# Kernel tuning notes

Measured on AMD Instinct MI355X. Metric: run time of the kernel, lower is better.

The kernel has to match this reference:

```python
import jax, jax.numpy as jnp
from jax import lax
import numpy as np

P, K1, K2 = 8, 5, 9  # nPaths, small/large ECA kernel sizes (from nDim=1024, nPaths=8)
LN_EPS = 1e-5


def setup_inputs() -> dict:
    key = jax.random.key(0)
    ks = jax.random.split(key, 6)
    b, c, l = 16, 1024, 4096
    return {
        "x": jax.random.normal(ks[0], (b, c, l), dtype=jnp.float32),
        "conv1_w": jax.random.normal(ks[1], (P, K1), dtype=jnp.float32) * 0.3,
        "conv2_w": jax.random.normal(ks[2], (P, K2), dtype=jnp.float32) * 0.3,
        "combine_w": jax.random.normal(ks[3], (2,), dtype=jnp.float32) * 0.5,
        "combine_b": jnp.zeros((), dtype=jnp.float32),
        "ln_g": jnp.ones((P,), dtype=jnp.float32),
        "ln_b": jnp.zeros((P,), dtype=jnp.float32),
        "W1": jax.random.normal(ks[4], (P, 2 * P), dtype=jnp.float32) * 0.3,
        "b1": jnp.zeros((2 * P,), dtype=jnp.float32),
        "W2": jax.random.normal(ks[5], (2 * P, P), dtype=jnp.float32) * 0.3,
        "b2": jnp.zeros((P,), dtype=jnp.float32),
    }


def _grouped_conv(y, w):
    # y: (b, P, D) pooled per-path features; w: (P, k) one 1-ch kernel per path.
    # Equivalent to the per-path Conv1d(1,1,k, padding=(k-1)//2) loop, fused.
    k = w.shape[-1]
    pad = (k - 1) // 2
    return lax.conv_general_dilated(
        y, w[:, None, :], window_strides=(1,), padding=[(pad, pad)],
        dimension_numbers=("NCH", "OIH", "NCH"), feature_group_count=y.shape[1])


def reference(x, conv1_w, conv2_w, combine_w, combine_b, ln_g, ln_b, W1, b1, W2, b2):
    b, c, l = x.shape
    nP = conv1_w.shape[0]
    D = c // nP
    pf = x.reshape(b, nP, D, l)          # (b, P, D, l)
    y = pf.mean(-1)                      # (b, P, D) global-avg-pool over l
    y1 = _grouped_conv(y, conv1_w)       # (b, P, D)
    y2 = _grouped_conv(y, conv2_w)       # (b, P, D)
    # combine = Conv1d(2,1,1): scalar mix of the two conv outputs + bias
    attn = jax.nn.sigmoid(combine_w[0] * y1 + combine_w[1] * y2 + combine_b)
    # cross-path gating MLP on per-path mean attention
    cross = attn.mean(-1)                # (b, P)
    mu = cross.mean(-1, keepdims=True)
    var = cross.var(-1, keepdims=True)   # biased, matches torch LayerNorm
    h = (cross - mu) / jnp.sqrt(var + LN_EPS) * ln_g + ln_b
    h = jax.nn.gelu(h @ W1 + b1, approximate=False)
    gate = jax.nn.sigmoid(h @ W2 + b2)   # (b, P)
    scale = attn * gate[:, :, None]      # (b, P, D)
    out = pf * scale[..., None]          # broadcast over l
    return out.reshape(b, c, l)
```

## Files before the change

kernel.cpp:

```cpp
#include <hip/hip_runtime.h>
#include <math.h>

#define NP 8
#define ND 128
#define NC 1024
#define NL 4096
#define NB 16
#define LN_EPS 1e-5f

#define NBLK 2048
#define NCHUNK 8
#define GRPS 64

typedef float v4f __attribute__((ext_vector_type(4)));

__device__ __forceinline__ float hsum(v4f v) { return v.x + v.y + v.z + v.w; }
__device__ __forceinline__ float sigmoid_f(float z) { return 1.f / (1.f + expf(-z)); }

__device__ __forceinline__ float gelu_f(float s) {
    const float t = 0.7978845608028654f * (s + 0.044715f * s * s * s);
    const float e = expf(2.f * t);
    return 0.5f * s * (1.f + (e - 1.f) / (e + 1.f));
}

__global__ __launch_bounds__(256, 8) void fused_kernel(
    const float* __restrict__ x, float* __restrict__ y,
    unsigned* __restrict__ garr, unsigned* __restrict__ root,
    const float* __restrict__ conv1_w, const float* __restrict__ conv2_w,
    const float* __restrict__ combine_w, const float* __restrict__ combine_b,
    const float* __restrict__ ln_g, const float* __restrict__ ln_b,
    const float* __restrict__ W1, const float* __restrict__ b1,
    const float* __restrict__ W2, const float* __restrict__ b2,
    float* __restrict__ out)
{
    const int tid = threadIdx.x;
    const int bid = blockIdx.x;
    const int grp = bid >> 5;

    __shared__ float sred[4];
    __shared__ float sy[NC];
    __shared__ float sattn[NC];
    __shared__ float scross[NP];
    __shared__ float sh[NP];
    __shared__ float sh2[2 * NP];
    __shared__ float sgate[NP];
    __shared__ float sml[2];

    for (int c = 0; c < NCHUNK; ++c) {
        const int rowc = c * NBLK + bid;
        const int b    = rowc >> 10;
        const int ch0  = rowc & (NC - 1);
        const v4f* xb  = (const v4f*)x + (size_t)rowc * (NL / 4);
        v4f* ob        = (v4f*)out    + (size_t)rowc * (NL / 4);

        v4f a0 = xb[tid], a1 = xb[tid + 256], a2 = xb[tid + 512], a3 = xb[tid + 768];
        {
            float ps = hsum(a0) + hsum(a1) + hsum(a2) + hsum(a3);
            ps += __shfl_down(ps, 32, 64); ps += __shfl_down(ps, 16, 64);
            ps += __shfl_down(ps, 8, 64);  ps += __shfl_down(ps, 4, 64);
            ps += __shfl_down(ps, 2, 64);  ps += __shfl_down(ps, 1, 64);
            if ((tid & 63) == 0) sred[tid >> 6] = ps;
        }
        __syncthreads();
        if (tid == 0) {
            y[rowc] = (sred[0] + sred[1] + sred[2] + sred[3]) * (1.f / NL);
            __threadfence();
            unsigned old = __hip_atomic_fetch_add(&garr[grp], 1u,
                              __ATOMIC_RELEASE, __HIP_MEMORY_SCOPE_AGENT);
            if (old == (unsigned)(c * 32 + 31))
                __hip_atomic_fetch_add(root, 1u,
                              __ATOMIC_RELEASE, __HIP_MEMORY_SCOPE_AGENT);
            while (__hip_atomic_load(root, __ATOMIC_ACQUIRE,
                                     __HIP_MEMORY_SCOPE_AGENT) < (unsigned)((c + 1) * GRPS))
                __builtin_amdgcn_s_sleep(2);
        }
        __syncthreads();

        const float* yb = y + b * NC;
        #pragma unroll
        for (int k = 0; k < 4; ++k) {
            const int i = tid + 256 * k;
            sy[i] = __hip_atomic_load(&yb[i], __ATOMIC_RELAXED, __HIP_MEMORY_SCOPE_AGENT);
        }
        __syncthreads();
        #pragma unroll
        for (int k = 0; k < 4; ++k) {
            const int pos = tid + 256 * k;
            const int p = pos >> 7, d = pos & 127;
            const float* rowp = sy + p * ND;
            float c1 = 0.f;
            #pragma unroll
            for (int t = 0; t < 5; ++t) {
                int dd = d + t - 2;
                float v = (dd >= 0 && dd < ND) ? rowp[dd] : 0.f;
                c1 += conv1_w[p * 5 + t] * v;
            }
            float c2 = 0.f;
            #pragma unroll
            for (int t = 0; t < 9; ++t) {
                int dd = d + t - 4;
                float v = (dd >= 0 && dd < ND) ? rowp[dd] : 0.f;
                c2 += conv2_w[p * 9 + t] * v;
            }
            sattn[pos] = sigmoid_f(combine_w[0] * c1 + combine_w[1] * c2 + combine_b[0]);
        }
        __syncthreads();
        if (tid < 128) {
            const int p = tid >> 4, o = (tid & 15) * 8;
            float s = 0.f;
            #pragma unroll
            for (int j = 0; j < 8; ++j) s += sattn[p * ND + o + j];
            s += __shfl_down(s, 8, 16); s += __shfl_down(s, 4, 16);
            s += __shfl_down(s, 2, 16); s += __shfl_down(s, 1, 16);
            if ((tid & 15) == 0) scross[p] = s * (1.f / ND);
        }
        __syncthreads();
        if (tid == 0) {
            float mu = 0.f;
            #pragma unroll
            for (int pp = 0; pp < NP; ++pp) mu += scross[pp];
            mu *= (1.f / NP);
            float var = 0.f;
            #pragma unroll
            for (int pp = 0; pp < NP; ++pp) { float dl = scross[pp] - mu; var += dl * dl; }
            sml[0] = mu;
            sml[1] = rsqrtf(var * (1.f / NP) + LN_EPS);
        }
        __syncthreads();
        if (tid < NP)
            sh[tid] = (scross[tid] - sml[0]) * sml[1] * ln_g[tid] + ln_b[tid];
        __syncthreads();
        if (tid < 2 * NP) {
            float s = b1[tid];
            #pragma unroll
            for (int pp = 0; pp < NP; ++pp) s += sh[pp] * W1[pp * (2 * NP) + tid];
            sh2[tid] = gelu_f(s);
        }
        __syncthreads();
        if (tid < NP) {
            float s = b2[tid];
            #pragma unroll
            for (int j = 0; j < 2 * NP; ++j) s += sh2[j] * W2[j * NP + tid];
            sgate[tid] = sigmoid_f(s);
        }
        __syncthreads();

        const float s = sattn[ch0] * sgate[ch0 >> 7];
        __builtin_nontemporal_store(a0 * s, &ob[tid]);
        __builtin_nontemporal_store(a1 * s, &ob[tid + 256]);
        __builtin_nontemporal_store(a2 * s, &ob[tid + 512]);
        __builtin_nontemporal_store(a3 * s, &ob[tid + 768]);
        __syncthreads();
    }
}

__global__ __launch_bounds__(256) void pool_kernel(const float* __restrict__ x,
                                                   float* __restrict__ y) {
    const int wid  = threadIdx.x >> 6;
    const int lane = threadIdx.x & 63;
    const int row  = blockIdx.x * 4 + wid;
    const v4f* xr = (const v4f*)(x + (size_t)row * NL);
    float s = 0.f;
    #pragma unroll
    for (int i = 0; i < 16; ++i) {
        v4f v = xr[lane + i * 64];
        s += v.x + v.y + v.z + v.w;
    }
    #pragma unroll
    for (int off = 32; off; off >>= 1) s += __shfl_down(s, off, 64);
    if (lane == 0) y[row] = s * (1.f / NL);
}

__global__ __launch_bounds__(1024) void attn_kernel(
    const float* __restrict__ y,
    const float* __restrict__ conv1_w, const float* __restrict__ conv2_w,
    const float* __restrict__ combine_w, const float* __restrict__ combine_b,
    const float* __restrict__ ln_g, const float* __restrict__ ln_b,
    const float* __restrict__ W1, const float* __restrict__ b1,
    const float* __restrict__ W2, const float* __restrict__ b2,
    float* __restrict__ scale)
{
    const int b = blockIdx.x;
    const int tid = threadIdx.x;
    const int p = tid >> 7;
    const int d = tid & 127;

    __shared__ float sy[NC];
    __shared__ float sattn[NC];
    __shared__ float sred[16];
    __shared__ float scross[NP];
    __shared__ float sh[NP];
    __shared__ float sh2[2 * NP];
    __shared__ float sgate[NP];
    __shared__ float sml[2];

    sy[tid] = y[b * NC + tid];
    __syncthreads();

    const float* rowp = sy + p * ND;
    float c1 = 0.f;
    #pragma unroll
    for (int t = 0; t < 5; ++t) {
        int dd = d + t - 2;
        float v = (dd >= 0 && dd < ND) ? rowp[dd] : 0.f;
        c1 += conv1_w[p * 5 + t] * v;
    }
    float c2 = 0.f;
    #pragma unroll
    for (int t = 0; t < 9; ++t) {
        int dd = d + t - 4;
        float v = (dd >= 0 && dd < ND) ? rowp[dd] : 0.f;
        c2 += conv2_w[p * 9 + t] * v;
    }
    const float a = sigmoid_f(combine_w[0] * c1 + combine_w[1] * c2 + combine_b[0]);
    sattn[tid] = a;

    float r = a;
    #pragma unroll
    for (int off = 32; off; off >>= 1) r += __shfl_down(r, off, 64);
    const int lane = tid & 63, wid = tid >> 6;
    if (lane == 0) sred[wid] = r;
    __syncthreads();

    if (tid == 0) {
        float mu = 0.f, var = 0.f;
        #pragma unroll
        for (int pp = 0; pp < NP; ++pp) {
            scross[pp] = (sred[2 * pp] + sred[2 * pp + 1]) * (1.f / ND);
            mu += scross[pp];
        }
        mu *= (1.f / NP);
        #pragma unroll
        for (int pp = 0; pp < NP; ++pp) { float dl = scross[pp] - mu; var += dl * dl; }
        sml[0] = mu;
        sml[1] = rsqrtf(var * (1.f / NP) + LN_EPS);
    }
    __syncthreads();
    if (tid < NP)
        sh[tid] = (scross[tid] - sml[0]) * sml[1] * ln_g[tid] + ln_b[tid];
    __syncthreads();
    if (tid < 2 * NP) {
        float s = b1[tid];
        #pragma unroll
        for (int pp = 0; pp < NP; ++pp) s += sh[pp] * W1[pp * (2 * NP) + tid];
        sh2[tid] = gelu_f(s);
    }
    __syncthreads();
    if (tid < NP) {
        float s = b2[tid];
        #pragma unroll
        for (int j = 0; j < 2 * NP; ++j) s += sh2[j] * W2[j * NP + tid];
        sgate[tid] = sigmoid_f(s);
    }
    __syncthreads();

    scale[b * NC + tid] = sattn[tid] * sgate[p];
}

__global__ __launch_bounds__(256) void scale_kernel(const float* __restrict__ x,
                                                    const float* __restrict__ scale,
                                                    float* __restrict__ out) {
    const v4f* xv = (const v4f*)x;
    v4f* ov = (v4f*)out;
    const size_t n = (size_t)NB * NC * (NL / 4);
    const size_t stride = (size_t)gridDim.x * blockDim.x;
    for (size_t i = (size_t)blockIdx.x * blockDim.x + threadIdx.x; i < n; i += stride) {
        const float s = scale[i >> 10];
        v4f v = xv[i];
        v *= s;
        __builtin_nontemporal_store(v, &ov[i]);
    }
}

extern "C" void kernel_launch(void* const* d_in, const int* in_sizes, int n_in,
                              void* d_out, int out_size, void* d_ws, size_t ws_size,
                              hipStream_t stream) {
    const float* x         = (const float*)d_in[0];
    const float* conv1_w   = (const float*)d_in[1];
    const float* conv2_w   = (const float*)d_in[2];
    const float* combine_w = (const float*)d_in[3];
    const float* combine_b = (const float*)d_in[4];
    const float* ln_g      = (const float*)d_in[5];
    const float* ln_b      = (const float*)d_in[6];
    const float* W1        = (const float*)d_in[7];
    const float* b1        = (const float*)d_in[8];
    const float* W2        = (const float*)d_in[9];
    const float* b2        = (const float*)d_in[10];
    float* out = (float*)d_out;

    float* y        = (float*)d_ws;
    float* scale    = y + NB * NC;
    unsigned* garr  = (unsigned*)(void*)(((char*)d_ws) + (NB * NC) * sizeof(float));
    unsigned* root  = garr + GRPS;

    hipMemsetAsync((void*)garr, 0, (GRPS + 16) * sizeof(unsigned), stream);

    int nb = 0;
    hipOccupancyMaxActiveBlocksPerMultiprocessor(&nb, fused_kernel, 256, 0);
    if (nb >= NBLK / 256) {
        void* args[] = { (void*)&x, (void*)&y, (void*)&garr, (void*)&root,
                         (void*)&conv1_w, (void*)&conv2_w,
                         (void*)&combine_w, (void*)&combine_b,
                         (void*)&ln_g, (void*)&ln_b,
                         (void*)&W1, (void*)&b1, (void*)&W2, (void*)&b2,
                         (void*)&out };
        hipLaunchCooperativeKernel((const void*)fused_kernel, dim3(NBLK), dim3(256),
                                   args, 0, stream);
    } else {
        pool_kernel<<<NB * NC / 4, 256, 0, stream>>>(x, y);
        attn_kernel<<<NB, 1024, 0, stream>>>(y, conv1_w, conv2_w, combine_w, combine_b,
                                             ln_g, ln_b, W1, b1, W2, b2, scale);
        scale_kernel<<<2048, 256, 0, stream>>>(x, scale, out);
    }
}
```

Baseline: 137.3 us.

## Prefetch next chunk across grid barrier and use hierarchical leader-based release

Loads the next chunk's input rows into registers before waiting on the grid-wide barrier, so the memory reads overlap the barrier wait. The barrier spin becomes two-level: only one leader block per group of 32 polls the root counter, then publishes a per-group release flag that the other blocks poll. This cuts contention on the single root atomic. The pooled-mean store becomes a relaxed atomic instead of store plus threadfence, and the loads now use relaxed ordering, which could weaken memory ordering guarantees. The extra prefetch registers could also reduce occupancy.

```diff
diff --git a/kernel.cpp b/kernel.cpp
--- a/kernel.cpp
+++ b/kernel.cpp
@@ -25,7 +25,8 @@
 
 __global__ __launch_bounds__(256, 8) void fused_kernel(
     const float* __restrict__ x, float* __restrict__ y,
-    unsigned* __restrict__ garr, unsigned* __restrict__ root,
+    unsigned* __restrict__ garr, unsigned* __restrict__ grel,
+    unsigned* __restrict__ root,
     const float* __restrict__ conv1_w, const float* __restrict__ conv2_w,
     const float* __restrict__ combine_w, const float* __restrict__ combine_b,
     const float* __restrict__ ln_g, const float* __restrict__ ln_b,
@@ -33,9 +34,10 @@
     const float* __restrict__ W2, const float* __restrict__ b2,
     float* __restrict__ out)
 {
-    const int tid = threadIdx.x;
-    const int bid = blockIdx.x;
-    const int grp = bid >> 5;
+    const int tid    = threadIdx.x;
+    const int bid    = blockIdx.x;
+    const int grp    = bid >> 5;
+    const bool lead  = (bid & 31) == 0;
 
     __shared__ float sred[4];
     __shared__ float sy[NC];
@@ -46,14 +48,19 @@
     __shared__ float sgate[NP];
     __shared__ float sml[2];
 
+    const size_t rstride = (size_t)NBLK * (NL / 4);
+
+    const v4f* xb = (const v4f*)x + (size_t)bid * (NL / 4);
+    v4f* ob       = (v4f*)out    + (size_t)bid * (NL / 4);
+
+    v4f a0 = xb[tid], a1 = xb[tid + 256], a2 = xb[tid + 512], a3 = xb[tid + 768];
+    v4f n0, n1, n2, n3;
+
     for (int c = 0; c < NCHUNK; ++c) {
         const int rowc = c * NBLK + bid;
         const int b    = rowc >> 10;
         const int ch0  = rowc & (NC - 1);
-        const v4f* xb  = (const v4f*)x + (size_t)rowc * (NL / 4);
-        v4f* ob        = (v4f*)out    + (size_t)rowc * (NL / 4);
-
-        v4f a0 = xb[tid], a1 = xb[tid + 256], a2 = xb[tid + 512], a3 = xb[tid + 768];
+
         {
             float ps = hsum(a0) + hsum(a1) + hsum(a2) + hsum(a3);
             ps += __shfl_down(ps, 32, 64); ps += __shfl_down(ps, 16, 64);
@@ -63,16 +70,32 @@
         }
         __syncthreads();
         if (tid == 0) {
-            y[rowc] = (sred[0] + sred[1] + sred[2] + sred[3]) * (1.f / NL);
-            __threadfence();
+            const float ym = (sred[0] + sred[1] + sred[2] + sred[3]) * (1.f / NL);
+            __hip_atomic_store(&y[rowc], ym, __ATOMIC_RELAXED, __HIP_MEMORY_SCOPE_AGENT);
             unsigned old = __hip_atomic_fetch_add(&garr[grp], 1u,
                               __ATOMIC_RELEASE, __HIP_MEMORY_SCOPE_AGENT);
             if (old == (unsigned)(c * 32 + 31))
                 __hip_atomic_fetch_add(root, 1u,
                               __ATOMIC_RELEASE, __HIP_MEMORY_SCOPE_AGENT);
-            while (__hip_atomic_load(root, __ATOMIC_ACQUIRE,
-                                     __HIP_MEMORY_SCOPE_AGENT) < (unsigned)((c + 1) * GRPS))
-                __builtin_amdgcn_s_sleep(2);
+        }
+
+        if (c + 1 < NCHUNK) {
+            const v4f* xn = xb + (size_t)(c + 1) * rstride;
+            n0 = xn[tid]; n1 = xn[tid + 256]; n2 = xn[tid + 512]; n3 = xn[tid + 768];
+        }
+
+        if (tid == 0) {
+            if (lead) {
+                while (__hip_atomic_load(root, __ATOMIC_RELAXED,
+                                         __HIP_MEMORY_SCOPE_AGENT) < (unsigned)((c + 1) * GRPS))
+                    __builtin_amdgcn_s_sleep(4);
+                __hip_atomic_store(&grel[grp], (unsigned)(c + 1),
+                                   __ATOMIC_RELAXED, __HIP_MEMORY_SCOPE_AGENT);
+            } else {
+                while (__hip_atomic_load(&grel[grp], __ATOMIC_RELAXED,
+                                         __HIP_MEMORY_SCOPE_AGENT) < (unsigned)(c + 1))
+                    __builtin_amdgcn_s_sleep(4);
+            }
         }
         __syncthreads();
 
@@ -145,11 +168,15 @@
         }
         __syncthreads();
 
-        const float s = sattn[ch0] * sgate[ch0 >> 7];
-        __builtin_nontemporal_store(a0 * s, &ob[tid]);
-        __builtin_nontemporal_store(a1 * s, &ob[tid + 256]);
-        __builtin_nontemporal_store(a2 * s, &ob[tid + 512]);
-        __builtin_nontemporal_store(a3 * s, &ob[tid + 768]);
+        {
+            const float s = sattn[ch0] * sgate[ch0 >> 7];
+            v4f* oc = ob + (size_t)c * rstride;
+            __builtin_nontemporal_store(a0 * s, &oc[tid]);
+            __builtin_nontemporal_store(a1 * s, &oc[tid + 256]);
+            __builtin_nontemporal_store(a2 * s, &oc[tid + 512]);
+            __builtin_nontemporal_store(a3 * s, &oc[tid + 768]);
+        }
+        a0 = n0; a1 = n1; a2 = n2; a3 = n3;
         __syncthreads();
     }
 }
@@ -290,15 +317,16 @@
 
     float* y        = (float*)d_ws;
     float* scale    = y + NB * NC;
-    unsigned* garr  = (unsigned*)(void*)(((char*)d_ws) + (NB * NC) * sizeof(float));
-    unsigned* root  = garr + GRPS;
-
-    hipMemsetAsync((void*)garr, 0, (GRPS + 16) * sizeof(unsigned), stream);
+    unsigned* garr  = (unsigned*)(void*)scale;
+    unsigned* grel  = garr + GRPS;
+    unsigned* root  = grel + GRPS;
+
+    hipMemsetAsync((void*)garr, 0, (2 * GRPS + 16) * sizeof(unsigned), stream);
 
     int nb = 0;
     hipOccupancyMaxActiveBlocksPerMultiprocessor(&nb, fused_kernel, 256, 0);
     if (nb >= NBLK / 256) {
-        void* args[] = { (void*)&x, (void*)&y, (void*)&garr, (void*)&root,
+        void* args[] = { (void*)&x, (void*)&y, (void*)&garr, (void*)&grel, (void*)&root,
                          (void*)&conv1_w, (void*)&conv2_w,
                          (void*)&combine_w, (void*)&combine_b,
                          (void*)&ln_g, (void*)&ln_b,
```

Result: no change. 135.3 us (-1.5%).
